# Kernel tuning notes

Hardware: AMD Instinct MI355X
Metric: run time of the kernel (lower is better)

## Reference

```python
import jax, jax.numpy as jnp
import numpy as np

MARGIN = 0.5
EPS = 1e-10


def setup_inputs() -> dict:
    key = jax.random.key(0)
    k1, k2 = jax.random.split(key)
    n, d = 8192, 256
    xs = jax.random.normal(k1, (n, d), dtype=jnp.float32)
    ys = jax.random.randint(k2, (n,), 0, 64, dtype=jnp.int64)
    return {"xs": xs, "ys": ys}


def reference(xs, ys):
    n = xs.shape[0]
    # pairwise squared L2: ||a||^2 + ||b||^2 - 2 a.b  -> [n, n]
    sq = jnp.sum(xs * xs, axis=1)
    dist2 = sq[:, None] + sq[None, :] - 2.0 * (xs @ xs.T)
    dist = jnp.sqrt(jnp.maximum(dist2, EPS))
    # same-label mask (includes diagonal, as in the original)
    mask = (ys[None, :] == ys[:, None]).astype(dist.dtype)  # [n, n]
    pos_cnt = jnp.sum(mask, axis=1)
    neg_cnt = n - pos_cnt
    dist_ap = jnp.sum(dist * mask, axis=1) / pos_cnt
    dist_an = jnp.sum(dist * (1.0 - mask), axis=1) / neg_cnt
    # MarginRankingLoss with y=1: mean(relu(-(dist_an - dist_ap) + margin))
    loss = jnp.mean(jnp.maximum(dist_ap - dist_an + MARGIN, 0.0))
    return loss
```

## Files before the change

### kernel.cpp

```cpp
#include <hip/hip_runtime.h>
#include <math.h>

#define N 8192
#define D 256
#define BK 32
#define TILE 128
#define NB (N / TILE)
#define NBLK (NB * (NB + 1) / 2)

typedef _Float16 half8 __attribute__((ext_vector_type(8)));
typedef float f32x4 __attribute__((ext_vector_type(4)));

constexpr float MARGIN = 0.5f;
constexpr float EPS_F  = 1e-10f;

__device__ inline void load_lds16(const void* g, void* l) {
    __builtin_amdgcn_global_load_lds(
        (const __attribute__((address_space(1))) void*)g,
        (__attribute__((address_space(3))) void*)l, 16, 0, 0);
}

__global__ void prep_kernel(const float* __restrict__ xs,
                            const int* __restrict__ ys_raw,
                            _Float16* __restrict__ x16, float* __restrict__ sq,
                            int* __restrict__ lbl, int* __restrict__ hist16,
                            float* __restrict__ sums, float* __restrict__ out) {
    const int tid = threadIdx.x;
    const int rb  = blockIdx.x;

    {
        const int r   = tid >> 4;
        const int c16 = tid & 15;
        const int row = rb * 16 + r;

        const float4* src = (const float4*)xs + (size_t)row * (D / 4) + c16 * 4;
        const float4 v0 = src[0], v1 = src[1], v2 = src[2], v3 = src[3];

        half8 h0 = { (_Float16)v0.x, (_Float16)v0.y, (_Float16)v0.z, (_Float16)v0.w,
                     (_Float16)v1.x, (_Float16)v1.y, (_Float16)v1.z, (_Float16)v1.w };
        half8 h1 = { (_Float16)v2.x, (_Float16)v2.y, (_Float16)v2.z, (_Float16)v2.w,
                     (_Float16)v3.x, (_Float16)v3.y, (_Float16)v3.z, (_Float16)v3.w };

        _Float16* dst = x16 + (size_t)row * D + c16 * 16;
        *(half8*)dst       = h0;
        *(half8*)(dst + 8) = h1;

        float s = v0.x*v0.x + v0.y*v0.y + v0.z*v0.z + v0.w*v0.w
                + v1.x*v1.x + v1.y*v1.y + v1.z*v1.z + v1.w*v1.w
                + v2.x*v2.x + v2.y*v2.y + v2.z*v2.z + v2.w*v2.w
                + v3.x*v3.x + v3.y*v3.y + v3.z*v3.z + v3.w*v3.w;
#pragma unroll
        for (int off = 1; off < 16; off <<= 1) s += __shfl_xor(s, off);
        if (c16 == 0) sq[row] = s;
    }

    if (rb < 16) {
        __shared__ int bad_s;
        __shared__ int lh[64];
        const int base = rb * 512;
        if (tid == 0) bad_s = 0;
        if (tid < 64) lh[tid] = 0;
        __syncthreads();
        int bad = 0;
        for (int i = tid; i < 512; i += 256) bad |= (ys_raw[2 * (base + i) + 1] != 0);
        if (bad) atomicOr(&bad_s, 1);
        __syncthreads();
        const bool is64 = (bad_s == 0);
        for (int i = tid; i < 512; i += 256) {
            const int v = is64 ? ys_raw[2 * (base + i)] : ys_raw[base + i];
            lbl[base + i] = v;
            atomicAdd(&lh[v & 63], 1);
        }
        __syncthreads();
        if (tid < 64) hist16[rb * 64 + tid] = lh[tid];
    }

    if (rb >= 16 && rb < 48) {
        const int base = (rb - 16) * 4096;
#pragma unroll
        for (int k = 0; k < 16; ++k) sums[base + k * 256 + tid] = 0.f;
    }
    if (rb == 48 && tid == 0) out[0] = 0.f;
}

__global__ __launch_bounds__(256, 3) void pair_kernel(
    const _Float16* __restrict__ x16, const int* __restrict__ lbl,
    const float* __restrict__ sq,
    float* __restrict__ sum_same8, float* __restrict__ sum_all8) {

    __shared__ _Float16 As[3][TILE * BK];
    __shared__ _Float16 Bs[3][TILE * BK];

    const int xcd = blockIdx.x & 7;
    const int t   = xcd * (NBLK / 8) + blockIdx.x / 8;
    float* __restrict__ sum_same = sum_same8 + (size_t)xcd * N;
    float* __restrict__ sum_all  = sum_all8  + (size_t)xcd * N;

    int bj = (int)((sqrtf(8.f * (float)t + 1.f) - 1.f) * 0.5f);
    while ((bj + 1) * (bj + 2) / 2 <= t) ++bj;
    while (bj * (bj + 1) / 2 > t) --bj;
    const int bi    = t - bj * (bj + 1) / 2;
    const bool diag = (bi == bj);
    const int i0 = bi * TILE;
    const int j0 = bj * TILE;

    const int tid  = threadIdx.x;
    const int w    = tid >> 6;
    const int lane = tid & 63;
    const int wm   = w >> 1;
    const int wn   = w & 1;
    const int cl   = lane & 15;
    const int g    = lane >> 4;

    f32x4 acc[4][4];
#pragma unroll
    for (int a = 0; a < 4; ++a)
#pragma unroll
        for (int b = 0; b < 4; ++b) acc[a][b] = (f32x4){0.f, 0.f, 0.f, 0.f};

    const int c0 = w * 64 + lane;
    const int r0 = c0 >> 2, kc0 = c0 & 3;
    const int c1 = 256 + c0;
    const int r1 = c1 >> 2, kc1 = c1 & 3;

#define STAGE(buf, k0)                                                          \
    do {                                                                        \
        load_lds16(x16 + (size_t)(i0 + r0) * D + (k0) + kc0 * 8,                \
                   &As[buf][(size_t)(w * 64) * 8]);                             \
        load_lds16(x16 + (size_t)(j0 + r0) * D + (k0) + kc0 * 8,                \
                   &Bs[buf][(size_t)(w * 64) * 8]);                             \
        load_lds16(x16 + (size_t)(i0 + r1) * D + (k0) + kc1 * 8,                \
                   &As[buf][(size_t)(256 + w * 64) * 8]);                       \
        load_lds16(x16 + (size_t)(j0 + r1) * D + (k0) + kc1 * 8,                \
                   &Bs[buf][(size_t)(256 + w * 64) * 8]);                       \
    } while (0)

    STAGE(0, 0);
    STAGE(1, BK);

    const int colbase = j0 + wn * 64;
    float sqj_[4];
    int   yj_[4];

#pragma unroll
    for (int t8 = 0; t8 < 8; ++t8) {
        const int cur = t8 % 3;

        if (t8 < 7) asm volatile("s_waitcnt vmcnt(4)" ::: "memory");
        else        asm volatile("s_waitcnt vmcnt(0)" ::: "memory");
        __builtin_amdgcn_s_barrier();

        if (t8 < 6) STAGE((t8 + 2) % 3, (t8 + 2) * BK);

        if (t8 == 7) {
#pragma unroll
            for (int nf = 0; nf < 4; ++nf) {
                const int c = colbase + nf * 16 + cl;
                sqj_[nf] = sq[c];
                yj_[nf]  = lbl[c];
            }
        }

        half8 af[4], bf[4];
#pragma unroll
        for (int mf = 0; mf < 4; ++mf)
            af[mf] = *(const half8*)&As[cur][(wm * 64 + mf * 16 + cl) * BK + g * 8];
#pragma unroll
        for (int nf = 0; nf < 4; ++nf)
            bf[nf] = *(const half8*)&Bs[cur][(wn * 64 + nf * 16 + cl) * BK + g * 8];

        __builtin_amdgcn_s_setprio(1);
#pragma unroll
        for (int mf = 0; mf < 4; ++mf)
#pragma unroll
            for (int nf = 0; nf < 4; ++nf)
                acc[mf][nf] = __builtin_amdgcn_mfma_f32_16x16x32_f16(
                    af[mf], bf[nf], acc[mf][nf], 0, 0, 0);
        __builtin_amdgcn_s_setprio(0);
    }
#undef STAGE

    const int rowbase = i0 + wm * 64;

    float cs_all[4], cs_same[4];
#pragma unroll
    for (int nf = 0; nf < 4; ++nf) { cs_all[nf] = 0.f; cs_same[nf] = 0.f; }

#pragma unroll
    for (int b = 0; b < 2; ++b) {
        float rs_all[8], rs_same[8];
#pragma unroll
        for (int e = 0; e < 8; ++e) { rs_all[e] = 0.f; rs_same[e] = 0.f; }

#pragma unroll
        for (int mh = 0; mh < 2; ++mh) {
            const int mf = 2 * b + mh;
#pragma unroll
            for (int r = 0; r < 4; ++r) {
                const int row   = rowbase + mf * 16 + g * 4 + r;
                const float sqi = sq[row];
                const int   yi  = lbl[row];
#pragma unroll
                for (int nf = 0; nf < 4; ++nf) {
                    float d2   = sqi + sqj_[nf] - 2.f * acc[mf][nf][r];
                    float dist = __builtin_amdgcn_sqrtf(fmaxf(d2, EPS_F));
                    if (diag) {
                        const int col = colbase + nf * 16 + cl;
                        if (row == col) dist = 1e-5f;
                    }
                    const float dm = (yi == yj_[nf]) ? dist : 0.f;
                    cs_all[nf] += dist;
                    cs_same[nf] += dm;
                    rs_all[mh * 4 + r] += dist;
                    rs_same[mh * 4 + r] += dm;
                }
            }
        }

        if (!diag) {
#define RSTEP(h, mask, bit)                                                     \
            {                                                                   \
                const bool hi = (cl >> (bit)) & 1;                              \
                _Pragma("unroll")                                               \
                for (int j = 0; j < (h); ++j) {                                 \
                    float sa_ = hi ? rs_all[j] : rs_all[j + (h)];               \
                    float ka_ = hi ? rs_all[j + (h)] : rs_all[j];               \
                    rs_all[j] = ka_ + __shfl_xor(sa_, (mask));                  \
                    float ss_ = hi ? rs_same[j] : rs_same[j + (h)];             \
                    float ks_ = hi ? rs_same[j + (h)] : rs_same[j];             \
                    rs_same[j] = ks_ + __shfl_xor(ss_, (mask));                 \
                }                                                               \
            }
            RSTEP(4, 8, 3)
            RSTEP(2, 4, 2)
            RSTEP(1, 2, 1)
#undef RSTEP
            rs_all[0]  += __shfl_xor(rs_all[0], 1);
            rs_same[0] += __shfl_xor(rs_same[0], 1);

            const int e    = cl >> 1;
            const int rrow = rowbase + (2 * b + (e >> 2)) * 16 + g * 4 + (e & 3);
            if (!(cl & 1)) {
                atomicAdd(&sum_all[rrow],  rs_all[0]);
                atomicAdd(&sum_same[rrow], rs_same[0]);
            }
        }
    }

    {
        const bool hi1 = (g >> 1) & 1;
#pragma unroll
        for (int j = 0; j < 2; ++j) {
            float sa_ = hi1 ? cs_all[j] : cs_all[j + 2];
            float ka_ = hi1 ? cs_all[j + 2] : cs_all[j];
            cs_all[j] = ka_ + __shfl_xor(sa_, 32);
            float ss_ = hi1 ? cs_same[j] : cs_same[j + 2];
            float ks_ = hi1 ? cs_same[j + 2] : cs_same[j];
            cs_same[j] = ks_ + __shfl_xor(ss_, 32);
        }
        const bool hi0 = g & 1;
        {
            float sa_ = hi0 ? cs_all[0] : cs_all[1];
            float ka_ = hi0 ? cs_all[1] : cs_all[0];
            cs_all[0] = ka_ + __shfl_xor(sa_, 16);
            float ss_ = hi0 ? cs_same[0] : cs_same[1];
            float ks_ = hi0 ? cs_same[1] : cs_same[0];
            cs_same[0] = ks_ + __shfl_xor(ss_, 16);
        }
        const int ccol = colbase + g * 16 + cl;
        atomicAdd(&sum_all[ccol],  cs_all[0]);
        atomicAdd(&sum_same[ccol], cs_same[0]);
    }
}

__global__ void finalize_kernel(const float* __restrict__ sum_same8,
                                const float* __restrict__ sum_all8,
                                const int* __restrict__ lbl,
                                const int* __restrict__ hist16,
                                float* __restrict__ out) {
    __shared__ int lh[64];
    __shared__ float wsums[4];
    const int tid = threadIdx.x;
    if (tid < 64) {
        int h = 0;
#pragma unroll
        for (int b = 0; b < 16; ++b) h += hist16[b * 64 + tid];
        lh[tid] = h;
    }
    __syncthreads();

    const int row = blockIdx.x * 256 + tid;
    float ss = 0.f, sa = 0.f;
#pragma unroll
    for (int x = 0; x < 8; ++x) {
        ss += sum_same8[(size_t)x * N + row];
        sa += sum_all8[(size_t)x * N + row];
    }

    const float cnt = (float)lh[lbl[row]];
    const float ap  = ss / cnt;
    const float an  = (sa - ss) / ((float)N - cnt);
    float local = fmaxf(ap - an + MARGIN, 0.f);

#pragma unroll
    for (int off = 32; off > 0; off >>= 1) local += __shfl_down(local, off);
    const int lane = tid & 63, wave = tid >> 6;
    if (lane == 0) wsums[wave] = local;
    __syncthreads();
    if (tid == 0)
        atomicAdd(out, (wsums[0] + wsums[1] + wsums[2] + wsums[3]) / (float)N);
}

extern "C" void kernel_launch(void* const* d_in, const int* in_sizes, int n_in,
                              void* d_out, int out_size, void* d_ws, size_t ws_size,
                              hipStream_t stream) {
    const float* xs     = (const float*)d_in[0];
    const int*   ys_raw = (const int*)d_in[1];

    float* ws        = (float*)d_ws;
    float* sum_same8 = ws;
    float* sum_all8  = ws + 8 * N;
    float* sqv       = ws + 16 * N;
    int*   lbl       = (int*)(ws + 17 * N);
    int*   hist16    = (int*)(ws + 18 * N);
    _Float16* x16    = (_Float16*)(ws + 18 * N + 1024);

    prep_kernel<<<N / 16, 256, 0, stream>>>(xs, ys_raw, x16, sqv, lbl, hist16,
                                            sum_same8, (float*)d_out);

    pair_kernel<<<NBLK, 256, 0, stream>>>(x16, lbl, sqv, sum_same8, sum_all8);

    finalize_kernel<<<32, 256, 0, stream>>>(sum_same8, sum_all8, lbl, hist16,
                                            (float*)d_out);
}
```

Baseline: 50.44 us.

## Pre-swizzle fp16 operands into MFMA fragment layout and load directly to registers

The prep kernel now writes the fp16 copy of xs in a blocked layout that matches the MFMA operand fragment order, so each lane's half8 is contiguous and coalesced. The pair kernel drops the LDS triple-buffered staging and barriers, loading A/B fragments straight from global memory into double-buffered registers. This removes LDS traffic and block-level syncs, but each wave now re-reads its operands from L2/global without sharing them through LDS, which raises global traffic and register pressure. The occupancy hint in launch bounds is also removed.

```diff
diff --git a/kernel.cpp b/kernel.cpp
--- a/kernel.cpp
+++ b/kernel.cpp
@@ -3,7 +3,6 @@
 
 #define N 8192
 #define D 256
-#define BK 32
 #define TILE 128
 #define NB (N / TILE)
 #define NBLK (NB * (NB + 1) / 2)
@@ -14,15 +13,10 @@
 constexpr float MARGIN = 0.5f;
 constexpr float EPS_F  = 1e-10f;
 
-__device__ inline void load_lds16(const void* g, void* l) {
-    __builtin_amdgcn_global_load_lds(
-        (const __attribute__((address_space(1))) void*)g,
-        (__attribute__((address_space(3))) void*)l, 16, 0, 0);
-}
 
 __global__ void prep_kernel(const float* __restrict__ xs,
                             const int* __restrict__ ys_raw,
-                            _Float16* __restrict__ x16, float* __restrict__ sq,
+                            _Float16* __restrict__ x16t, float* __restrict__ sq,
                             int* __restrict__ lbl, int* __restrict__ hist16,
                             float* __restrict__ sums, float* __restrict__ out) {
     const int tid = threadIdx.x;
@@ -41,9 +35,9 @@
         half8 h1 = { (_Float16)v2.x, (_Float16)v2.y, (_Float16)v2.z, (_Float16)v2.w,
                      (_Float16)v3.x, (_Float16)v3.y, (_Float16)v3.z, (_Float16)v3.w };
 
-        _Float16* dst = x16 + (size_t)row * D + c16 * 16;
-        *(half8*)dst       = h0;
-        *(half8*)(dst + 8) = h1;
+        _Float16* dst = x16t + (size_t)rb * 4096 + (c16 * 2) * 128 + r * 8;
+        *(half8*)dst         = h0;
+        *(half8*)(dst + 128) = h1;
 
         float s = v0.x*v0.x + v0.y*v0.y + v0.z*v0.z + v0.w*v0.w
                 + v1.x*v1.x + v1.y*v1.y + v1.z*v1.z + v1.w*v1.w
@@ -83,13 +77,10 @@
     if (rb == 48 && tid == 0) out[0] = 0.f;
 }
 
-__global__ __launch_bounds__(256, 3) void pair_kernel(
-    const _Float16* __restrict__ x16, const int* __restrict__ lbl,
+__global__ __launch_bounds__(256) void pair_kernel(
+    const _Float16* __restrict__ x16t, const int* __restrict__ lbl,
     const float* __restrict__ sq,
     float* __restrict__ sum_same8, float* __restrict__ sum_all8) {
-
-    __shared__ _Float16 As[3][TILE * BK];
-    __shared__ _Float16 Bs[3][TILE * BK];
 
     const int xcd = blockIdx.x & 7;
     const int t   = xcd * (NBLK / 8) + blockIdx.x / 8;
@@ -118,25 +109,15 @@
 #pragma unroll
         for (int b = 0; b < 4; ++b) acc[a][b] = (f32x4){0.f, 0.f, 0.f, 0.f};
 
-    const int c0 = w * 64 + lane;
-    const int r0 = c0 >> 2, kc0 = c0 & 3;
-    const int c1 = 256 + c0;
-    const int r1 = c1 >> 2, kc1 = c1 & 3;
-
-#define STAGE(buf, k0)                                                          \
-    do {                                                                        \
-        load_lds16(x16 + (size_t)(i0 + r0) * D + (k0) + kc0 * 8,                \
-                   &As[buf][(size_t)(w * 64) * 8]);                             \
-        load_lds16(x16 + (size_t)(j0 + r0) * D + (k0) + kc0 * 8,                \
-                   &Bs[buf][(size_t)(w * 64) * 8]);                             \
-        load_lds16(x16 + (size_t)(i0 + r1) * D + (k0) + kc1 * 8,                \
-                   &As[buf][(size_t)(256 + w * 64) * 8]);                       \
-        load_lds16(x16 + (size_t)(j0 + r1) * D + (k0) + kc1 * 8,                \
-                   &Bs[buf][(size_t)(256 + w * 64) * 8]);                       \
-    } while (0)
-
-    STAGE(0, 0);
-    STAGE(1, BK);
+    const _Float16* pa = x16t + (size_t)((i0 >> 4) + wm * 4) * 4096 + g * 128 + cl * 8;
+    const _Float16* pb = x16t + (size_t)((j0 >> 4) + wn * 4) * 4096 + g * 128 + cl * 8;
+
+    half8 af[2][4], bf[2][4];
+#pragma unroll
+    for (int mf = 0; mf < 4; ++mf) {
+        af[0][mf] = *(const half8*)(pa + mf * 4096);
+        bf[0][mf] = *(const half8*)(pb + mf * 4096);
+    }
 
     const int colbase = j0 + wn * 64;
     float sqj_[4];
@@ -144,14 +125,14 @@
 
 #pragma unroll
     for (int t8 = 0; t8 < 8; ++t8) {
-        const int cur = t8 % 3;
-
-        if (t8 < 7) asm volatile("s_waitcnt vmcnt(4)" ::: "memory");
-        else        asm volatile("s_waitcnt vmcnt(0)" ::: "memory");
-        __builtin_amdgcn_s_barrier();
-
-        if (t8 < 6) STAGE((t8 + 2) % 3, (t8 + 2) * BK);
-
+        if (t8 < 7) {
+            const int koff = (t8 + 1) * 512;
+#pragma unroll
+            for (int mf = 0; mf < 4; ++mf) {
+                af[(t8 + 1) & 1][mf] = *(const half8*)(pa + mf * 4096 + koff);
+                bf[(t8 + 1) & 1][mf] = *(const half8*)(pb + mf * 4096 + koff);
+            }
+        }
         if (t8 == 7) {
 #pragma unroll
             for (int nf = 0; nf < 4; ++nf) {
@@ -161,24 +142,15 @@
             }
         }
 
-        half8 af[4], bf[4];
-#pragma unroll
-        for (int mf = 0; mf < 4; ++mf)
-            af[mf] = *(const half8*)&As[cur][(wm * 64 + mf * 16 + cl) * BK + g * 8];
-#pragma unroll
-        for (int nf = 0; nf < 4; ++nf)
-            bf[nf] = *(const half8*)&Bs[cur][(wn * 64 + nf * 16 + cl) * BK + g * 8];
-
         __builtin_amdgcn_s_setprio(1);
 #pragma unroll
         for (int mf = 0; mf < 4; ++mf)
 #pragma unroll
             for (int nf = 0; nf < 4; ++nf)
                 acc[mf][nf] = __builtin_amdgcn_mfma_f32_16x16x32_f16(
-                    af[mf], bf[nf], acc[mf][nf], 0, 0, 0);
+                    af[t8 & 1][mf], bf[t8 & 1][nf], acc[mf][nf], 0, 0, 0);
         __builtin_amdgcn_s_setprio(0);
     }
-#undef STAGE
 
     const int rowbase = i0 + wm * 64;
 
@@ -323,12 +295,12 @@
     float* sqv       = ws + 16 * N;
     int*   lbl       = (int*)(ws + 17 * N);
     int*   hist16    = (int*)(ws + 18 * N);
-    _Float16* x16    = (_Float16*)(ws + 18 * N + 1024);
-
-    prep_kernel<<<N / 16, 256, 0, stream>>>(xs, ys_raw, x16, sqv, lbl, hist16,
+    _Float16* x16t   = (_Float16*)(ws + 18 * N + 1024);
+
+    prep_kernel<<<N / 16, 256, 0, stream>>>(xs, ys_raw, x16t, sqv, lbl, hist16,
                                             sum_same8, (float*)d_out);
 
-    pair_kernel<<<NBLK, 256, 0, stream>>>(x16, lbl, sqv, sum_same8, sum_all8);
+    pair_kernel<<<NBLK, 256, 0, stream>>>(x16t, lbl, sqv, sum_same8, sum_all8);
 
     finalize_kernel<<<32, 256, 0, stream>>>(sum_same8, sum_all8, lbl, hist16,
                                             (float*)d_out);
```

Measured after the change: 50.37 us. No clear change (-0.1%).

## Process two adjacent column tiles per block with cross-tile prefetch

Applied to the files above, without the earlier changes.

Each block now handles a strip of up to two horizontally adjacent 128x128 tiles in the upper triangle, reducing the grid from 2080 to 1056 blocks. The second tile's B loads are issued during the last k-steps of the first tile, so its pipeline starts warm, and the first tile's atomics are deferred until after the second tile's compute. This is meant to cut per-block launch and prologue overhead and hide the pipeline fill latency, at the cost of longer blocks, more live registers for the held epilogue results, and a coarser tail with fewer blocks.

```diff
diff --git a/kernel.cpp b/kernel.cpp
--- a/kernel.cpp
+++ b/kernel.cpp
@@ -6,7 +6,7 @@
 #define BK 32
 #define TILE 128
 #define NB (N / TILE)
-#define NBLK (NB * (NB + 1) / 2)
+#define NSTRIP 1056
 
 typedef _Float16 half8 __attribute__((ext_vector_type(8)));
 typedef float f32x4 __attribute__((ext_vector_type(4)));
@@ -83,108 +83,18 @@
     if (rb == 48 && tid == 0) out[0] = 0.f;
 }
 
-__global__ __launch_bounds__(256, 3) void pair_kernel(
-    const _Float16* __restrict__ x16, const int* __restrict__ lbl,
-    const float* __restrict__ sq,
-    float* __restrict__ sum_same8, float* __restrict__ sum_all8) {
-
-    __shared__ _Float16 As[3][TILE * BK];
-    __shared__ _Float16 Bs[3][TILE * BK];
-
-    const int xcd = blockIdx.x & 7;
-    const int t   = xcd * (NBLK / 8) + blockIdx.x / 8;
-    float* __restrict__ sum_same = sum_same8 + (size_t)xcd * N;
-    float* __restrict__ sum_all  = sum_all8  + (size_t)xcd * N;
-
-    int bj = (int)((sqrtf(8.f * (float)t + 1.f) - 1.f) * 0.5f);
-    while ((bj + 1) * (bj + 2) / 2 <= t) ++bj;
-    while (bj * (bj + 1) / 2 > t) --bj;
-    const int bi    = t - bj * (bj + 1) / 2;
-    const bool diag = (bi == bj);
-    const int i0 = bi * TILE;
-    const int j0 = bj * TILE;
-
-    const int tid  = threadIdx.x;
-    const int w    = tid >> 6;
-    const int lane = tid & 63;
-    const int wm   = w >> 1;
-    const int wn   = w & 1;
-    const int cl   = lane & 15;
-    const int g    = lane >> 4;
-
-    f32x4 acc[4][4];
-#pragma unroll
-    for (int a = 0; a < 4; ++a)
-#pragma unroll
-        for (int b = 0; b < 4; ++b) acc[a][b] = (f32x4){0.f, 0.f, 0.f, 0.f};
-
-    const int c0 = w * 64 + lane;
-    const int r0 = c0 >> 2, kc0 = c0 & 3;
-    const int c1 = 256 + c0;
-    const int r1 = c1 >> 2, kc1 = c1 & 3;
-
-#define STAGE(buf, k0)                                                          \
-    do {                                                                        \
-        load_lds16(x16 + (size_t)(i0 + r0) * D + (k0) + kc0 * 8,                \
-                   &As[buf][(size_t)(w * 64) * 8]);                             \
-        load_lds16(x16 + (size_t)(j0 + r0) * D + (k0) + kc0 * 8,                \
-                   &Bs[buf][(size_t)(w * 64) * 8]);                             \
-        load_lds16(x16 + (size_t)(i0 + r1) * D + (k0) + kc1 * 8,                \
-                   &As[buf][(size_t)(256 + w * 64) * 8]);                       \
-        load_lds16(x16 + (size_t)(j0 + r1) * D + (k0) + kc1 * 8,                \
-                   &Bs[buf][(size_t)(256 + w * 64) * 8]);                       \
-    } while (0)
-
-    STAGE(0, 0);
-    STAGE(1, BK);
-
-    const int colbase = j0 + wn * 64;
-    float sqj_[4];
-    int   yj_[4];
-
-#pragma unroll
-    for (int t8 = 0; t8 < 8; ++t8) {
-        const int cur = t8 % 3;
-
-        if (t8 < 7) asm volatile("s_waitcnt vmcnt(4)" ::: "memory");
-        else        asm volatile("s_waitcnt vmcnt(0)" ::: "memory");
-        __builtin_amdgcn_s_barrier();
-
-        if (t8 < 6) STAGE((t8 + 2) % 3, (t8 + 2) * BK);
-
-        if (t8 == 7) {
-#pragma unroll
-            for (int nf = 0; nf < 4; ++nf) {
-                const int c = colbase + nf * 16 + cl;
-                sqj_[nf] = sq[c];
-                yj_[nf]  = lbl[c];
-            }
-        }
-
-        half8 af[4], bf[4];
-#pragma unroll
-        for (int mf = 0; mf < 4; ++mf)
-            af[mf] = *(const half8*)&As[cur][(wm * 64 + mf * 16 + cl) * BK + g * 8];
-#pragma unroll
-        for (int nf = 0; nf < 4; ++nf)
-            bf[nf] = *(const half8*)&Bs[cur][(wn * 64 + nf * 16 + cl) * BK + g * 8];
-
-        __builtin_amdgcn_s_setprio(1);
-#pragma unroll
-        for (int mf = 0; mf < 4; ++mf)
-#pragma unroll
-            for (int nf = 0; nf < 4; ++nf)
-                acc[mf][nf] = __builtin_amdgcn_mfma_f32_16x16x32_f16(
-                    af[mf], bf[nf], acc[mf][nf], 0, 0, 0);
-        __builtin_amdgcn_s_setprio(0);
-    }
-#undef STAGE
-
-    const int rowbase = i0 + wm * 64;
-
+struct EpiOut { float ca, cs, ra0, rs0, ra1, rs1; };
+
+__device__ __forceinline__ EpiOut tile_epilogue(
+    const f32x4 (&acc)[4][4], const float* __restrict__ sq,
+    const int* __restrict__ lbl, const float (&sqj_)[4], const int (&yj_)[4],
+    int rowbase, int colbase, bool diag, int cl, int g) {
+
+    EpiOut o;
     float cs_all[4], cs_same[4];
 #pragma unroll
     for (int nf = 0; nf < 4; ++nf) { cs_all[nf] = 0.f; cs_same[nf] = 0.f; }
+    float rout_a[2], rout_s[2];
 
 #pragma unroll
     for (int b = 0; b < 2; ++b) {
@@ -217,35 +127,30 @@
             }
         }
 
-        if (!diag) {
 #define RSTEP(h, mask, bit)                                                     \
-            {                                                                   \
-                const bool hi = (cl >> (bit)) & 1;                              \
-                _Pragma("unroll")                                               \
-                for (int j = 0; j < (h); ++j) {                                 \
-                    float sa_ = hi ? rs_all[j] : rs_all[j + (h)];               \
-                    float ka_ = hi ? rs_all[j + (h)] : rs_all[j];               \
-                    rs_all[j] = ka_ + __shfl_xor(sa_, (mask));                  \
-                    float ss_ = hi ? rs_same[j] : rs_same[j + (h)];             \
-                    float ks_ = hi ? rs_same[j + (h)] : rs_same[j];             \
-                    rs_same[j] = ks_ + __shfl_xor(ss_, (mask));                 \
-                }                                                               \
-            }
-            RSTEP(4, 8, 3)
-            RSTEP(2, 4, 2)
-            RSTEP(1, 2, 1)
+        {                                                                       \
+            const bool hi = (cl >> (bit)) & 1;                                  \
+            _Pragma("unroll")                                                   \
+            for (int j = 0; j < (h); ++j) {                                     \
+                float sa_ = hi ? rs_all[j] : rs_all[j + (h)];                   \
+                float ka_ = hi ? rs_all[j + (h)] : rs_all[j];                   \
+                rs_all[j] = ka_ + __shfl_xor(sa_, (mask));                      \
+                float ss_ = hi ? rs_same[j] : rs_same[j + (h)];                 \
+                float ks_ = hi ? rs_same[j + (h)] : rs_same[j];                 \
+                rs_same[j] = ks_ + __shfl_xor(ss_, (mask));                     \
+            }                                                                   \
+        }
+        RSTEP(4, 8, 3)
+        RSTEP(2, 4, 2)
+        RSTEP(1, 2, 1)
 #undef RSTEP
-            rs_all[0]  += __shfl_xor(rs_all[0], 1);
-            rs_same[0] += __shfl_xor(rs_same[0], 1);
-
-            const int e    = cl >> 1;
-            const int rrow = rowbase + (2 * b + (e >> 2)) * 16 + g * 4 + (e & 3);
-            if (!(cl & 1)) {
-                atomicAdd(&sum_all[rrow],  rs_all[0]);
-                atomicAdd(&sum_same[rrow], rs_same[0]);
-            }
-        }
-    }
+        rs_all[0]  += __shfl_xor(rs_all[0], 1);
+        rs_same[0] += __shfl_xor(rs_same[0], 1);
+        rout_a[b] = rs_all[0];
+        rout_s[b] = rs_same[0];
+    }
+    o.ra0 = rout_a[0]; o.rs0 = rout_s[0];
+    o.ra1 = rout_a[1]; o.rs1 = rout_s[1];
 
     {
         const bool hi1 = (g >> 1) & 1;
@@ -259,18 +164,196 @@
             cs_same[j] = ks_ + __shfl_xor(ss_, 32);
         }
         const bool hi0 = g & 1;
-        {
-            float sa_ = hi0 ? cs_all[0] : cs_all[1];
-            float ka_ = hi0 ? cs_all[1] : cs_all[0];
-            cs_all[0] = ka_ + __shfl_xor(sa_, 16);
-            float ss_ = hi0 ? cs_same[0] : cs_same[1];
-            float ks_ = hi0 ? cs_same[1] : cs_same[0];
-            cs_same[0] = ks_ + __shfl_xor(ss_, 16);
-        }
-        const int ccol = colbase + g * 16 + cl;
-        atomicAdd(&sum_all[ccol],  cs_all[0]);
-        atomicAdd(&sum_same[ccol], cs_same[0]);
-    }
+        float sa_ = hi0 ? cs_all[0] : cs_all[1];
+        float ka_ = hi0 ? cs_all[1] : cs_all[0];
+        o.ca = ka_ + __shfl_xor(sa_, 16);
+        float ss_ = hi0 ? cs_same[0] : cs_same[1];
+        float ks_ = hi0 ? cs_same[1] : cs_same[0];
+        o.cs = ks_ + __shfl_xor(ss_, 16);
+    }
+    return o;
+}
+
+__device__ __forceinline__ void fire_atomics(
+    const EpiOut& o, float* __restrict__ sum_all, float* __restrict__ sum_same,
+    int rowbase, int colbase, bool diag, int cl, int g) {
+    if (!diag && !(cl & 1)) {
+        const int e = cl >> 1;
+        const int r0 = rowbase + (e >> 2) * 16 + g * 4 + (e & 3);
+        atomicAdd(&sum_all[r0],  o.ra0);
+        atomicAdd(&sum_same[r0], o.rs0);
+        const int r1 = rowbase + (2 + (e >> 2)) * 16 + g * 4 + (e & 3);
+        atomicAdd(&sum_all[r1],  o.ra1);
+        atomicAdd(&sum_same[r1], o.rs1);
+    }
+    const int ccol = colbase + g * 16 + cl;
+    atomicAdd(&sum_all[ccol],  o.ca);
+    atomicAdd(&sum_same[ccol], o.cs);
+}
+
+__global__ __launch_bounds__(256, 3) void pair_kernel(
+    const _Float16* __restrict__ x16, const int* __restrict__ lbl,
+    const float* __restrict__ sq,
+    float* __restrict__ sum_same8, float* __restrict__ sum_all8) {
+
+    __shared__ _Float16 As[3][TILE * BK];
+    __shared__ _Float16 Bs[3][TILE * BK];
+
+    const int xcd = blockIdx.x & 7;
+    int rem = xcd * (NSTRIP / 8) + blockIdx.x / 8;
+    float* __restrict__ sum_same = sum_same8 + (size_t)xcd * N;
+    float* __restrict__ sum_all  = sum_all8  + (size_t)xcd * N;
+
+    int bi = 0;
+    for (;;) {
+        const int ns = (65 - bi) >> 1;
+        if (rem < ns) break;
+        rem -= ns;
+        ++bi;
+    }
+    const int bj0   = bi + 2 * rem;
+    const int npan  = (bj0 == 63) ? 1 : 2;
+    const bool diag0 = (bj0 == bi);
+    const int i0 = bi * TILE;
+
+    const int tid  = threadIdx.x;
+    const int w    = tid >> 6;
+    const int lane = tid & 63;
+    const int wm   = w >> 1;
+    const int wn   = w & 1;
+    const int cl   = lane & 15;
+    const int g    = lane >> 4;
+
+    const int rowbase  = i0 + wm * 64;
+    const int colbase0 = bj0 * TILE + wn * 64;
+    const int colbase1 = (bj0 + 1) * TILE + wn * 64;
+
+    f32x4 acc[4][4];
+#pragma unroll
+    for (int a = 0; a < 4; ++a)
+#pragma unroll
+        for (int b = 0; b < 4; ++b) acc[a][b] = (f32x4){0.f, 0.f, 0.f, 0.f};
+
+    const int c0 = w * 64 + lane;
+    const int r0 = c0 >> 2, kc0 = c0 & 3;
+    const int c1 = 256 + c0;
+    const int r1 = c1 >> 2, kc1 = c1 & 3;
+
+#define STAGE(buf, jbase, k0)                                                   \
+    do {                                                                        \
+        load_lds16(x16 + (size_t)(i0 + r0) * D + (k0) + kc0 * 8,                \
+                   &As[buf][(size_t)(w * 64) * 8]);                             \
+        load_lds16(x16 + (size_t)((jbase) + r0) * D + (k0) + kc0 * 8,           \
+                   &Bs[buf][(size_t)(w * 64) * 8]);                             \
+        load_lds16(x16 + (size_t)(i0 + r1) * D + (k0) + kc1 * 8,                \
+                   &As[buf][(size_t)(256 + w * 64) * 8]);                       \
+        load_lds16(x16 + (size_t)((jbase) + r1) * D + (k0) + kc1 * 8,           \
+                   &Bs[buf][(size_t)(256 + w * 64) * 8]);                       \
+    } while (0)
+
+    STAGE(0, bj0 * TILE, 0);
+    STAGE(1, bj0 * TILE, BK);
+
+    float sqj_[4];
+    int   yj_[4];
+    EpiOut ep0;
+
+#pragma unroll
+    for (int t8 = 0; t8 < 8; ++t8) {
+        const int cur = t8 % 3;
+
+        if (t8 < 7)          asm volatile("s_waitcnt vmcnt(4)" ::: "memory");
+        else if (npan == 2)  asm volatile("s_waitcnt vmcnt(4)" ::: "memory");
+        else                 asm volatile("s_waitcnt vmcnt(0)" ::: "memory");
+        __builtin_amdgcn_s_barrier();
+
+        if (t8 < 6) {
+            STAGE((t8 + 2) % 3, bj0 * TILE, (t8 + 2) * BK);
+        } else if (npan == 2) {
+            STAGE((t8 + 2) % 3, (bj0 + 1) * TILE, (t8 - 6) * BK);
+        }
+
+        if (t8 == 7) {
+#pragma unroll
+            for (int nf = 0; nf < 4; ++nf) {
+                const int c = colbase0 + nf * 16 + cl;
+                sqj_[nf] = sq[c];
+                yj_[nf]  = lbl[c];
+            }
+        }
+
+        half8 af[4], bf[4];
+#pragma unroll
+        for (int mf = 0; mf < 4; ++mf)
+            af[mf] = *(const half8*)&As[cur][(wm * 64 + mf * 16 + cl) * BK + g * 8];
+#pragma unroll
+        for (int nf = 0; nf < 4; ++nf)
+            bf[nf] = *(const half8*)&Bs[cur][(wn * 64 + nf * 16 + cl) * BK + g * 8];
+
+        __builtin_amdgcn_s_setprio(1);
+#pragma unroll
+        for (int mf = 0; mf < 4; ++mf)
+#pragma unroll
+            for (int nf = 0; nf < 4; ++nf)
+                acc[mf][nf] = __builtin_amdgcn_mfma_f32_16x16x32_f16(
+                    af[mf], bf[nf], acc[mf][nf], 0, 0, 0);
+        __builtin_amdgcn_s_setprio(0);
+    }
+
+    if (npan == 1) {
+        ep0 = tile_epilogue(acc, sq, lbl, sqj_, yj_, rowbase, colbase0, diag0, cl, g);
+        fire_atomics(ep0, sum_all, sum_same, rowbase, colbase0, diag0, cl, g);
+        return;
+    }
+
+    ep0 = tile_epilogue(acc, sq, lbl, sqj_, yj_, rowbase, colbase0, diag0, cl, g);
+
+#pragma unroll
+    for (int a = 0; a < 4; ++a)
+#pragma unroll
+        for (int b = 0; b < 4; ++b) acc[a][b] = (f32x4){0.f, 0.f, 0.f, 0.f};
+
+#pragma unroll
+    for (int ks = 0; ks < 8; ++ks) {
+        const int cur = (ks + 2) % 3;
+
+        if (ks < 7) asm volatile("s_waitcnt vmcnt(4)" ::: "memory");
+        else        asm volatile("s_waitcnt vmcnt(0)" ::: "memory");
+        __builtin_amdgcn_s_barrier();
+
+        if (ks < 6) STAGE((ks + 1) % 3, (bj0 + 1) * TILE, (ks + 2) * BK);
+
+        if (ks == 7) {
+#pragma unroll
+            for (int nf = 0; nf < 4; ++nf) {
+                const int c = colbase1 + nf * 16 + cl;
+                sqj_[nf] = sq[c];
+                yj_[nf]  = lbl[c];
+            }
+        }
+
+        half8 af[4], bf[4];
+#pragma unroll
+        for (int mf = 0; mf < 4; ++mf)
+            af[mf] = *(const half8*)&As[cur][(wm * 64 + mf * 16 + cl) * BK + g * 8];
+#pragma unroll
+        for (int nf = 0; nf < 4; ++nf)
+            bf[nf] = *(const half8*)&Bs[cur][(wn * 64 + nf * 16 + cl) * BK + g * 8];
+
+        __builtin_amdgcn_s_setprio(1);
+#pragma unroll
+        for (int mf = 0; mf < 4; ++mf)
+#pragma unroll
+            for (int nf = 0; nf < 4; ++nf)
+                acc[mf][nf] = __builtin_amdgcn_mfma_f32_16x16x32_f16(
+                    af[mf], bf[nf], acc[mf][nf], 0, 0, 0);
+        __builtin_amdgcn_s_setprio(0);
+    }
+#undef STAGE
+
+    EpiOut ep1 = tile_epilogue(acc, sq, lbl, sqj_, yj_, rowbase, colbase1, false, cl, g);
+    fire_atomics(ep1, sum_all, sum_same, rowbase, colbase1, false, cl, g);
+    fire_atomics(ep0, sum_all, sum_same, rowbase, colbase0, diag0, cl, g);
 }
 
 __global__ void finalize_kernel(const float* __restrict__ sum_same8,
@@ -328,7 +411,7 @@
     prep_kernel<<<N / 16, 256, 0, stream>>>(xs, ys_raw, x16, sqv, lbl, hist16,
                                             sum_same8, (float*)d_out);
 
-    pair_kernel<<<NBLK, 256, 0, stream>>>(x16, lbl, sqv, sum_same8, sum_all8);
+    pair_kernel<<<NSTRIP, 256, 0, stream>>>(x16, lbl, sqv, sum_same8, sum_all8);
 
     finalize_kernel<<<32, 256, 0, stream>>>(sum_same8, sum_all8, lbl, hist16,
                                             (float*)d_out);
```

Measured after the change: 94.69 us. 1.88x slower.
